# Kernel tuning notes

Hardware: AMD Instinct MI355X
Metric: run time of the kernel (lower is better)

The kernel has to match this reference:

```python
import jax, jax.numpy as jnp
import numpy as np
import math

B, D, C = 2048, 128, 50000
NUM_IDS = 512
ARC_MARGIN, ARC_SCALE = 0.5, 64.0
COS_M, SIN_M = math.cos(ARC_MARGIN), math.sin(ARC_MARGIN)
TH = math.cos(math.pi - ARC_MARGIN)
MM = math.sin(math.pi - ARC_MARGIN) * ARC_MARGIN
LABEL_SMOOTH = 0.1
TRIPLET_MARGIN = 0.3
W_ARC, W_TRI = 1.0, 0.5
BIG = 1e9


def setup_inputs() -> dict:
    key = jax.random.key(0)
    k1, k2, k3 = jax.random.split(key, 3)
    embeddings = jax.random.normal(k1, (B, D), dtype=jnp.float32)
    # xavier-uniform init of nn.Linear(D, C, bias=False).weight -> [C, D]
    limit = math.sqrt(6.0 / (C + D))
    arcface_weight_mat = jax.random.uniform(k2, (C, D), minval=-limit, maxval=limit, dtype=jnp.float32)
    labels = jax.random.randint(k3, (B,), 0, NUM_IDS, dtype=jnp.int64)
    return {"embeddings": embeddings, "arcface_weight_mat": arcface_weight_mat, "labels": labels}


def _arcface_loss(emb, W, labels):
    emb_n = emb / jnp.linalg.norm(emb, axis=1, keepdims=True)
    w_n = W / jnp.linalg.norm(W, axis=1, keepdims=True)
    cosine = emb_n @ w_n.T                                   # [B, C]
    sine = jnp.sqrt(jnp.clip(1.0 - cosine * cosine, 0.0, 1.0))
    phi = cosine * COS_M - sine * SIN_M                      # cos(theta + m)
    phi = jnp.where(cosine > TH, phi, cosine - MM)           # easy-margin fallback
    onehot = jax.nn.one_hot(labels, C, dtype=cosine.dtype)
    logits = ARC_SCALE * (onehot * phi + (1.0 - onehot) * cosine)
    logp = jax.nn.log_softmax(logits, axis=1)
    nll = -jnp.take_along_axis(logp, labels[:, None], axis=1)[:, 0]
    smooth = -logp.mean(axis=1)
    return ((1.0 - LABEL_SMOOTH) * nll + LABEL_SMOOTH * smooth).mean()


def _batch_hard_triplet(emb, labels):
    dot = emb @ emb.T                                        # [B, B]
    sq = jnp.diagonal(dot)
    dist = jnp.sqrt(jax.nn.relu(sq[None, :] - 2.0 * dot + sq[:, None]) + 1e-16)
    same = (labels[:, None] == labels[None, :]).astype(emb.dtype)
    eye = jnp.eye(labels.shape[0], dtype=emb.dtype)
    pos_mask = same - eye
    hardest_pos = (dist * pos_mask).max(axis=1)
    hardest_neg = (dist + pos_mask * BIG + eye * BIG).min(axis=1)
    loss = jax.nn.relu(hardest_pos - hardest_neg + TRIPLET_MARGIN)
    valid = (pos_mask.sum(axis=1) > 0).astype(emb.dtype)
    n_valid = valid.sum()
    return jnp.where(n_valid > 0, (loss * valid).sum() / jnp.maximum(n_valid, 1.0), 0.0)


def reference(embeddings, arcface_weight_mat, labels):
    arc = _arcface_loss(embeddings, arcface_weight_mat, labels)
    tri = _batch_hard_triplet(embeddings, labels)
    return W_ARC * arc + W_TRI * tri
```

## Files before the change

### kernel.cpp

```cpp
#include <hip/hip_runtime.h>
#include <math.h>

#define Bn 2048
#define Dd 128
#define Cc 50000
#define NSPL 24
#define NTILE 782
#define TS 32

#define COS_Mf 0.8775825618903728f
#define SIN_Mf 0.479425538604203f
#define THf (-0.8775825618903728f)
#define MMf 0.2397127693021015f
#define L2E64 92.33248261689366f

typedef __attribute__((ext_vector_type(8))) short short8;
typedef __attribute__((ext_vector_type(4))) float f32x4;

__device__ __forceinline__ unsigned short f2bf(float f) {
    unsigned int u = __float_as_uint(f);
    u += 0x7fffu + ((u >> 16) & 1u);
    return (unsigned short)(u >> 16);
}
__device__ __forceinline__ float bf2f(unsigned short h) {
    return __uint_as_float(((unsigned int)h) << 16);
}

__global__ void norm_all(const float* __restrict__ emb, const float* __restrict__ W,
                         unsigned short* __restrict__ embn, unsigned short* __restrict__ rawb,
                         float* __restrict__ sqn, unsigned short* __restrict__ wnb,
                         float* __restrict__ zp) {
    if (blockIdx.x == 0) zp[threadIdx.x] = 0.f;
    int wid = threadIdx.x >> 6;
    int lane = threadIdx.x & 63;
    int half = lane >> 5, l32 = lane & 31;
    int row = blockIdx.x * 8 + wid * 2 + half;
    bool ise = row < Bn;
    int r = ise ? row : row - Bn;
    const float* p = (ise ? emb : W) + (size_t)r * Dd + l32 * 4;
    float4 v = *reinterpret_cast<const float4*>(p);
    float ss = v.x * v.x + v.y * v.y + v.z * v.z + v.w * v.w;
    #pragma unroll
    for (int o = 16; o > 0; o >>= 1) ss += __shfl_xor(ss, o);
    float rn = rsqrtf(ss);
    ushort4 q4 = make_ushort4(f2bf(v.x * rn), f2bf(v.y * rn), f2bf(v.z * rn), f2bf(v.w * rn));
    *reinterpret_cast<ushort4*>((ise ? embn : wnb) + (size_t)r * Dd + l32 * 4) = q4;
    if (ise) {
        ushort4 r4 = make_ushort4(f2bf(v.x), f2bf(v.y), f2bf(v.z), f2bf(v.w));
        *reinterpret_cast<ushort4*>(rawb + (size_t)r * Dd + l32 * 4) = r4;
        if (l32 == 0) sqn[r] = ss;
    }
}

struct AuxS { float s[16][128]; };
struct TripS { unsigned short swt[8192]; float red[128][2][3]; };

__launch_bounds__(256, 2)
__global__ void mid_k(const unsigned short* __restrict__ embn,
                      const unsigned short* __restrict__ wnb,
                      const int* __restrict__ lab,
                      float* __restrict__ esum, float* __restrict__ wsum,
                      float* __restrict__ bx, float* __restrict__ tg,
                      const unsigned short* __restrict__ eb, const float* __restrict__ sqn,
                      float* __restrict__ hp, float* __restrict__ hn,
                      float* __restrict__ cnt) {
    __shared__ __align__(16) char smem[sizeof(TripS)];
    const int bid = blockIdx.x;
    const int t = threadIdx.x;

    if (bid < 784) {
        AuxS& S = *reinterpret_cast<AuxS*>(smem);
        if (bid < 272) {
            int rg = t >> 4;
            int cg = (t & 15) * 8;
            const unsigned short* src;
            float* dst;
            int r0, rend;
            if (bid < 256) {
                src = wnb; dst = wsum;
                r0 = bid * 196;
                rend = r0 + 196; if (rend > Cc) rend = Cc;
            } else {
                src = embn; dst = esum;
                r0 = (bid - 256) * 128;
                rend = r0 + 128;
            }
            float acc[8];
            #pragma unroll
            for (int j = 0; j < 8; ++j) acc[j] = 0.f;
            for (int r = r0 + rg; r < rend; r += 16) {
                short8 v = *reinterpret_cast<const short8*>(src + (size_t)r * Dd + cg);
                #pragma unroll
                for (int j = 0; j < 8; ++j) acc[j] += bf2f((unsigned short)v[j]);
            }
            #pragma unroll
            for (int j = 0; j < 8; ++j) S.s[rg][cg + j] = acc[j];
            __syncthreads();
            if (t < 128) {
                float v = 0.f;
                #pragma unroll
                for (int u = 0; u < 16; ++u) v += S.s[u][t];
                atomicAdd(&dst[t], v);
            }
        } else {
            int wid = t >> 6, lane = t & 63;
            int row = (bid - 272) * 4 + wid;
            int lb = lab[row];
            const unsigned short* e = embn + (size_t)row * Dd;
            const unsigned short* wv = wnb + (size_t)lb * Dd;
            float sv = bf2f(e[lane]) * bf2f(wv[lane]) + bf2f(e[lane + 64]) * bf2f(wv[lane + 64]);
            #pragma unroll
            for (int o = 32; o > 0; o >>= 1) sv += __shfl_xor(sv, o);
            if (lane == 0) {
                float c = sv;
                float s2 = fminf(fmaxf(1.f - c * c, 0.f), 1.f);
                float sine = sqrtf(s2);
                float phi = c * COS_Mf - sine * SIN_Mf;
                phi = (c > THf) ? phi : (c - MMf);
                bx[row] = 64.f * c;
                tg[row] = 64.f * phi;
            }
        }
    } else {
        TripS& S = *reinterpret_cast<TripS*>(smem);
        const int tb = bid - 784;
        const int w = t >> 6, l = t & 63;
        const int r0 = (tb & 15) * 128;
        const int split = tb >> 4;
        const int c0 = split * 64;
        const int rowbase = r0 + (w & 1) * 64;
        const int colb = (w >> 1) * 32;

        #pragma unroll
        for (int j = 0; j < 4; ++j) {
            int col = (w * 4 + j) * 4 + (l >> 4);
            int kb = ((l & 15) * 16) ^ ((col & 7) << 4);
            const unsigned short* src = eb + ((size_t)(c0 + col) << 7) + (kb >> 1);
            __builtin_amdgcn_global_load_lds(
                (const __attribute__((address_space(1))) void*)src,
                (__attribute__((address_space(3))) void*)(&S.swt[(w * 4 + j) * 512]),
                16, 0, 0);
        }

        short8 afrag[4][4];
        #pragma unroll
        for (int sm = 0; sm < 4; ++sm)
            #pragma unroll
            for (int kc = 0; kc < 4; ++kc) {
                int row = rowbase + sm * 16 + (l & 15);
                int k0 = kc * 32 + (l >> 4) * 8;
                afrag[sm][kc] = *reinterpret_cast<const short8*>(eb + (size_t)row * Dd + k0);
            }

        float rsq[4][4]; int rlb[4][4];
        #pragma unroll
        for (int sm = 0; sm < 4; ++sm)
            #pragma unroll
            for (int r = 0; r < 4; ++r) {
                int row = rowbase + sm * 16 + (l >> 4) * 4 + r;
                rsq[sm][r] = sqn[row];
                rlb[sm][r] = lab[row];
            }
        int cj[2]; float csq[2]; int clb[2];
        #pragma unroll
        for (int sn = 0; sn < 2; ++sn) {
            cj[sn] = c0 + colb + sn * 16 + (l & 15);
            csq[sn] = sqn[cj[sn]];
            clb[sn] = lab[cj[sn]];
        }

        __syncthreads();

        f32x4 acc[4][2];
        #pragma unroll
        for (int sm = 0; sm < 4; ++sm)
            #pragma unroll
            for (int sn = 0; sn < 2; ++sn)
                acc[sm][sn] = (f32x4){0.f, 0.f, 0.f, 0.f};

        #pragma unroll
        for (int kc = 0; kc < 4; ++kc) {
            short8 bfr[2];
            #pragma unroll
            for (int sn = 0; sn < 2; ++sn) {
                int rcol = colb + sn * 16 + (l & 15);
                int rkb = (kc * 64 + (l >> 4) * 16) ^ ((rcol & 7) << 4);
                bfr[sn] = *reinterpret_cast<const short8*>(S.swt + rcol * 128 + (rkb >> 1));
            }
            #pragma unroll
            for (int sn = 0; sn < 2; ++sn)
                #pragma unroll
                for (int sm = 0; sm < 4; ++sm)
                    acc[sm][sn] = __builtin_amdgcn_mfma_f32_16x16x32_bf16(
                        afrag[sm][kc], bfr[sn], acc[sm][sn], 0, 0, 0);
        }

        float vhp[4][4], vhn[4][4], vct[4][4];
        #pragma unroll
        for (int sm = 0; sm < 4; ++sm)
            #pragma unroll
            for (int r = 0; r < 4; ++r) { vhp[sm][r] = 0.f; vhn[sm][r] = 1e30f; vct[sm][r] = 0.f; }

        #pragma unroll
        for (int sm = 0; sm < 4; ++sm)
            #pragma unroll
            for (int r = 0; r < 4; ++r) {
                int rg = rowbase + sm * 16 + (l >> 4) * 4 + r;
                #pragma unroll
                for (int sn = 0; sn < 2; ++sn) {
                    float d2 = fmaf(acc[sm][sn][r], -2.f, rsq[sm][r] + csq[sn]);
                    float dist = sqrtf(fmaxf(d2, 0.f) + 1e-16f);
                    bool same = (rlb[sm][r] == clb[sn]);
                    bool psel = same && (rg != cj[sn]);
                    if (psel) { vhp[sm][r] = fmaxf(vhp[sm][r], dist); vct[sm][r] += 1.f; }
                    if (!same) vhn[sm][r] = fminf(vhn[sm][r], dist);
                }
            }

        #pragma unroll
        for (int sm = 0; sm < 4; ++sm)
            #pragma unroll
            for (int r = 0; r < 4; ++r) {
                float a = vhp[sm][r], b = vhn[sm][r], c = vct[sm][r];
                #pragma unroll
                for (int o = 1; o < 16; o <<= 1) {
                    a = fmaxf(a, __shfl_xor(a, o));
                    b = fminf(b, __shfl_xor(b, o));
                    c += __shfl_xor(c, o);
                }
                if ((l & 15) == 0) {
                    int row = (w & 1) * 64 + sm * 16 + (l >> 4) * 4 + r;
                    S.red[row][w >> 1][0] = a;
                    S.red[row][w >> 1][1] = b;
                    S.red[row][w >> 1][2] = c;
                }
            }
        __syncthreads();
        if (t < 128) {
            float a = fmaxf(S.red[t][0][0], S.red[t][1][0]);
            float b = fminf(S.red[t][0][1], S.red[t][1][1]);
            float c = S.red[t][0][2] + S.red[t][1][2];
            hp[(size_t)split * Bn + r0 + t] = a;
            hn[(size_t)split * Bn + r0 + t] = b;
            cnt[(size_t)split * Bn + r0 + t] = c;
        }
    }
}

__launch_bounds__(256, 3)
__global__ void arc_main(const unsigned short* __restrict__ en,
                         const unsigned short* __restrict__ wn,
                         float* __restrict__ ps) {
    __shared__ unsigned short swb[4][3][2048];
    __shared__ float sred[4][64];
    const int t = threadIdx.x;
    const int w = t >> 6, l = t & 63;
    const int id = blockIdx.x;
    const int xcd = id & 7, j = id >> 3;
    const int r0 = (j / 3) * 64;
    const int split = xcd * 3 + (j % 3);
    const int strip = w * 16;
    const int lc = l & 15, lk = l >> 4;

    short8 afrag[4][4];
    #pragma unroll
    for (int sm = 0; sm < 4; ++sm)
        #pragma unroll
        for (int kc = 0; kc < 4; ++kc)
            afrag[sm][kc] = *reinterpret_cast<const short8*>(
                en + (size_t)(r0 + sm * 16 + lc) * Dd + kc * 32 + lk * 8);

    float sacc[4][4];
    #pragma unroll
    for (int sm = 0; sm < 4; ++sm)
        #pragma unroll
        for (int r = 0; r < 4; ++r) sacc[sm][r] = 0.f;

    const int ntm = (NTILE - 1 - split) / NSPL + 1;

    size_t loff[4];
    #pragma unroll
    for (int jj = 0; jj < 4; ++jj) {
        int colloc = jj * 4 + lk;
        int kb = (lc * 16) ^ ((colloc & 7) << 4);
        loff[jj] = ((size_t)(strip + colloc) << 7) + (kb >> 1);
    }

    auto STAGE = [&](unsigned short* buf, int idx) {
        int tl = split + idx * NSPL;
        if (tl > NTILE - 1) tl = NTILE - 1;
        const unsigned short* tb = wn + ((size_t)tl << 13);
        #pragma unroll
        for (int jj = 0; jj < 4; ++jj) {
            __builtin_amdgcn_global_load_lds(
                (const __attribute__((address_space(1))) void*)(tb + loff[jj]),
                (__attribute__((address_space(3))) void*)(buf + jj * 512),
                16, 0, 0);
        }
    };

    unsigned short* b0 = &swb[w][0][0];
    unsigned short* b1 = &swb[w][1][0];
    unsigned short* b2 = &swb[w][2][0];

    STAGE(b0, 0);
    STAGE(b1, 1);
    STAGE(b2, 2);

#define ASTEP(BUF, I) {                                                        \
    if ((I) < ntm) {                                                           \
        asm volatile("s_waitcnt vmcnt(8)" ::: "memory");                       \
        short8 bfr[4];                                                         \
        _Pragma("unroll")                                                      \
        for (int kc = 0; kc < 4; ++kc) {                                       \
            int rkb = (kc * 64 + lk * 16) ^ ((lc & 7) << 4);                   \
            bfr[kc] = *reinterpret_cast<const short8*>(BUF + lc * 128 + (rkb >> 1)); \
        }                                                                      \
        asm volatile("s_waitcnt lgkmcnt(0)" ::: "memory");                     \
        STAGE(BUF, (I) + 3);                                                   \
        f32x4 acc[4];                                                          \
        _Pragma("unroll")                                                      \
        for (int sm = 0; sm < 4; ++sm) acc[sm] = (f32x4){0.f, 0.f, 0.f, 0.f};  \
        _Pragma("unroll")                                                      \
        for (int kc = 0; kc < 4; ++kc)                                         \
            _Pragma("unroll")                                                  \
            for (int sm = 0; sm < 4; ++sm)                                     \
                acc[sm] = __builtin_amdgcn_mfma_f32_16x16x32_bf16(             \
                    afrag[sm][kc], bfr[kc], acc[sm], 0, 0, 0);                 \
        const int c0t = (split + (I) * NSPL) * 64;                             \
        if (c0t + strip < Cc) {                                                \
            _Pragma("unroll")                                                  \
            for (int sm = 0; sm < 4; ++sm)                                     \
                _Pragma("unroll")                                              \
                for (int r = 0; r < 4; ++r)                                    \
                    sacc[sm][r] += __builtin_amdgcn_exp2f(                     \
                        fmaf(acc[sm][r], L2E64, -L2E64));                      \
        }                                                                      \
    } }

    for (int ii = 0; ii < 33; ii += 3) {
        ASTEP(b0, ii);
        ASTEP(b1, ii + 1);
        ASTEP(b2, ii + 2);
    }
#undef ASTEP

    #pragma unroll
    for (int sm = 0; sm < 4; ++sm)
        #pragma unroll
        for (int r = 0; r < 4; ++r) {
            float v = sacc[sm][r];
            v += __shfl_xor(v, 1); v += __shfl_xor(v, 2);
            v += __shfl_xor(v, 4); v += __shfl_xor(v, 8);
            sacc[sm][r] = v;
        }
    if (lc == 0) {
        #pragma unroll
        for (int sm = 0; sm < 4; ++sm)
            #pragma unroll
            for (int r = 0; r < 4; ++r)
                sred[w][sm * 16 + lk * 4 + r] = sacc[sm][r];
    }
    __syncthreads();
    if (t < 64) {
        float sv = sred[0][t] + sred[1][t] + sred[2][t] + sred[3][t];
        ps[(size_t)split * Bn + r0 + t] = sv;
    }
}

__launch_bounds__(256)
__global__ void final_k(const float* __restrict__ ps, const float* __restrict__ bx,
                        const float* __restrict__ tg, const float* __restrict__ hp,
                        const float* __restrict__ hn, const float* __restrict__ cnt,
                        float* __restrict__ gpart) {
    __shared__ float sA[4], sT[4], sV[4];
    int t = threadIdx.x;
    int row = blockIdx.x * 64 + (t >> 2);
    int part = t & 3;
    float s = 0.f;
    for (int u = part; u < NSPL; u += 4) s += ps[(size_t)u * Bn + row];
    float a = 0.f, b = 1e30f, c = 0.f;
    for (int u = part; u < TS; u += 4) {
        a = fmaxf(a, hp[(size_t)u * Bn + row]);
        b = fminf(b, hn[(size_t)u * Bn + row]);
        c += cnt[(size_t)u * Bn + row];
    }
    s += __shfl_xor(s, 1); s += __shfl_xor(s, 2);
    a = fmaxf(a, __shfl_xor(a, 1)); a = fmaxf(a, __shfl_xor(a, 2));
    b = fminf(b, __shfl_xor(b, 1)); b = fminf(b, __shfl_xor(b, 2));
    c += __shfl_xor(c, 1); c += __shfl_xor(c, 2);

    float arcs = 0.f, tris = 0.f, vals = 0.f;
    if (part == 0) {
        float base = bx[row], targ = tg[row];
        s += __expf(targ - 64.f) - __expf(base - 64.f);
        float lse = 64.f + logf(s);
        arcs = lse - 0.9f * targ - 0.1f * (targ - base) / (float)Cc;
        float tl = fmaxf(a - b + 0.3f, 0.f);
        tris = (c > 0.f) ? tl : 0.f;
        vals = (c > 0.f) ? 1.f : 0.f;
    }

    #pragma unroll
    for (int o = 32; o > 0; o >>= 1) {
        arcs += __shfl_xor(arcs, o);
        tris += __shfl_xor(tris, o);
        vals += __shfl_xor(vals, o);
    }
    int wid = t >> 6, lane = t & 63;
    if (lane == 0) { sA[wid] = arcs; sT[wid] = tris; sV[wid] = vals; }
    __syncthreads();
    if (t == 0) {
        gpart[blockIdx.x * 3 + 0] = sA[0] + sA[1] + sA[2] + sA[3];
        gpart[blockIdx.x * 3 + 1] = sT[0] + sT[1] + sT[2] + sT[3];
        gpart[blockIdx.x * 3 + 2] = sV[0] + sV[1] + sV[2] + sV[3];
    }
}

__global__ void final2_k(const float* __restrict__ gpart, const float* __restrict__ es,
                         const float* __restrict__ wsum, float* __restrict__ out) {
    int l = threadIdx.x;
    float x = es[l] * wsum[l] + es[l + 64] * wsum[l + 64];
    #pragma unroll
    for (int o = 32; o > 0; o >>= 1) x += __shfl_xor(x, o);
    if (l == 0) {
        float A = 0.f, T = 0.f, V = 0.f;
        for (int b = 0; b < 32; ++b) {
            A += gpart[b * 3 + 0];
            T += gpart[b * 3 + 1];
            V += gpart[b * 3 + 2];
        }
        float tri = (V > 0.f) ? (T / fmaxf(V, 1.f)) : 0.f;
        out[0] = (A - 6.4f * x / (float)Cc) / (float)Bn + 0.5f * tri;
    }
}

extern "C" void kernel_launch(void* const* d_in, const int* in_sizes, int n_in,
                              void* d_out, int out_size, void* d_ws, size_t ws_size,
                              hipStream_t stream) {
    const float* emb = (const float*)d_in[0];
    const float* W = (const float*)d_in[1];
    const int* lab = (const int*)d_in[2];
    float* out = (float*)d_out;

    unsigned short* embn = (unsigned short*)d_ws;
    unsigned short* rawb = embn + (size_t)Bn * Dd;
    unsigned short* wnb = rawb + (size_t)Bn * Dd;
    float* sqn = (float*)(wnb + (size_t)Cc * Dd);
    float* ps = sqn + Bn;
    float* bx = ps + (size_t)NSPL * Bn;
    float* tg = bx + Bn;
    float* hp = tg + Bn;
    float* hn = hp + (size_t)TS * Bn;
    float* ct = hn + (size_t)TS * Bn;
    float* esum = ct + (size_t)TS * Bn;
    float* wsum = esum + 128;
    float* gpart = wsum + 128;

    norm_all<<<256 + Cc / 8, 256, 0, stream>>>(emb, W, embn, rawb, sqn, wnb, esum);
    mid_k<<<784 + 512, 256, 0, stream>>>(embn, wnb, lab, esum, wsum, bx, tg,
                                         rawb, sqn, hp, hn, ct);
    arc_main<<<768, 256, 0, stream>>>(embn, wnb, ps);
    final_k<<<32, 256, 0, stream>>>(ps, bx, tg, hp, hn, ct, gpart);
    final2_k<<<1, 64, 0, stream>>>(gpart, esum, wsum, out);
}
```

Baseline: 71.85 us.

## Fold final reduction into final_k via last-block atomic and raise MFMA priority

Removes the separate single-block final2_k launch by having each final_k block bump an atomic counter, so the last block to finish does the global reduction and writes the output. The counter is reset in norm_all. MFMA sections in arc_main are also wrapped in s_setprio(1)/s_setprio(0) to favour the matrix issue over other waves. This saves one kernel launch and its gap, at the cost of a threadfence and an atomic per block.

```diff
diff --git a/kernel.cpp b/kernel.cpp
--- a/kernel.cpp
+++ b/kernel.cpp
@@ -29,8 +29,11 @@
 __global__ void norm_all(const float* __restrict__ emb, const float* __restrict__ W,
                          unsigned short* __restrict__ embn, unsigned short* __restrict__ rawb,
                          float* __restrict__ sqn, unsigned short* __restrict__ wnb,
-                         float* __restrict__ zp) {
-    if (blockIdx.x == 0) zp[threadIdx.x] = 0.f;
+                         float* __restrict__ zp, unsigned int* __restrict__ done_ct) {
+    if (blockIdx.x == 0) {
+        zp[threadIdx.x] = 0.f;
+        if (threadIdx.x == 0) *done_ct = 0u;
+    }
     int wid = threadIdx.x >> 6;
     int lane = threadIdx.x & 63;
     int half = lane >> 5, l32 = lane & 31;
@@ -321,12 +324,14 @@
         f32x4 acc[4];                                                          \
         _Pragma("unroll")                                                      \
         for (int sm = 0; sm < 4; ++sm) acc[sm] = (f32x4){0.f, 0.f, 0.f, 0.f};  \
+        __builtin_amdgcn_s_setprio(1);                                         \
         _Pragma("unroll")                                                      \
         for (int kc = 0; kc < 4; ++kc)                                         \
             _Pragma("unroll")                                                  \
             for (int sm = 0; sm < 4; ++sm)                                     \
                 acc[sm] = __builtin_amdgcn_mfma_f32_16x16x32_bf16(             \
                     afrag[sm][kc], bfr[kc], acc[sm], 0, 0, 0);                 \
+        __builtin_amdgcn_s_setprio(0);                                         \
         const int c0t = (split + (I) * NSPL) * 64;                             \
         if (c0t + strip < Cc) {                                                \
             _Pragma("unroll")                                                  \
@@ -372,8 +377,11 @@
 __global__ void final_k(const float* __restrict__ ps, const float* __restrict__ bx,
                         const float* __restrict__ tg, const float* __restrict__ hp,
                         const float* __restrict__ hn, const float* __restrict__ cnt,
-                        float* __restrict__ gpart) {
+                        float* __restrict__ gpart, unsigned int* __restrict__ done_ct,
+                        const float* __restrict__ es, const float* __restrict__ wsum,
+                        float* __restrict__ out) {
     __shared__ float sA[4], sT[4], sV[4];
+    __shared__ int lastf;
     int t = threadIdx.x;
     int row = blockIdx.x * 64 + (t >> 2);
     int part = t & 3;
@@ -414,24 +422,33 @@
         gpart[blockIdx.x * 3 + 0] = sA[0] + sA[1] + sA[2] + sA[3];
         gpart[blockIdx.x * 3 + 1] = sT[0] + sT[1] + sT[2] + sT[3];
         gpart[blockIdx.x * 3 + 2] = sV[0] + sV[1] + sV[2] + sV[3];
-    }
-}
-
-__global__ void final2_k(const float* __restrict__ gpart, const float* __restrict__ es,
-                         const float* __restrict__ wsum, float* __restrict__ out) {
-    int l = threadIdx.x;
-    float x = es[l] * wsum[l] + es[l + 64] * wsum[l + 64];
-    #pragma unroll
-    for (int o = 32; o > 0; o >>= 1) x += __shfl_xor(x, o);
-    if (l == 0) {
+        __threadfence();
+        unsigned int old = atomicAdd(done_ct, 1u);
+        lastf = (old == 31u) ? 1 : 0;
+    }
+    __syncthreads();
+    if (lastf && t < 64) {
+        __threadfence();
+        int l = t;
+        float x = es[l] * wsum[l] + es[l + 64] * wsum[l + 64];
+        #pragma unroll
+        for (int o = 32; o > 0; o >>= 1) x += __shfl_xor(x, o);
         float A = 0.f, T = 0.f, V = 0.f;
-        for (int b = 0; b < 32; ++b) {
-            A += gpart[b * 3 + 0];
-            T += gpart[b * 3 + 1];
-            V += gpart[b * 3 + 2];
-        }
-        float tri = (V > 0.f) ? (T / fmaxf(V, 1.f)) : 0.f;
-        out[0] = (A - 6.4f * x / (float)Cc) / (float)Bn + 0.5f * tri;
+        if (l < 32) {
+            A = gpart[l * 3 + 0];
+            T = gpart[l * 3 + 1];
+            V = gpart[l * 3 + 2];
+        }
+        #pragma unroll
+        for (int o = 32; o > 0; o >>= 1) {
+            A += __shfl_xor(A, o);
+            T += __shfl_xor(T, o);
+            V += __shfl_xor(V, o);
+        }
+        if (l == 0) {
+            float tri = (V > 0.f) ? (T / fmaxf(V, 1.f)) : 0.f;
+            out[0] = (A - 6.4f * x / (float)Cc) / (float)Bn + 0.5f * tri;
+        }
     }
 }
 
@@ -456,11 +473,12 @@
     float* esum = ct + (size_t)TS * Bn;
     float* wsum = esum + 128;
     float* gpart = wsum + 128;
-
-    norm_all<<<256 + Cc / 8, 256, 0, stream>>>(emb, W, embn, rawb, sqn, wnb, esum);
+    unsigned int* done_ct = (unsigned int*)(gpart + 96);
+
+    norm_all<<<256 + Cc / 8, 256, 0, stream>>>(emb, W, embn, rawb, sqn, wnb, esum, done_ct);
     mid_k<<<784 + 512, 256, 0, stream>>>(embn, wnb, lab, esum, wsum, bx, tg,
                                          rawb, sqn, hp, hn, ct);
     arc_main<<<768, 256, 0, stream>>>(embn, wnb, ps);
-    final_k<<<32, 256, 0, stream>>>(ps, bx, tg, hp, hn, ct, gpart);
-    final2_k<<<1, 64, 0, stream>>>(gpart, esum, wsum, out);
-}
+    final_k<<<32, 256, 0, stream>>>(ps, bx, tg, hp, hn, ct, gpart, done_ct,
+                                    esum, wsum, out);
+}
```

After: 71.05 us (median of 2 runs). No clear change (-1.1%).
